# Optimization experiments

Measured on AMD Instinct MI355X. Metric: run time of the kernel, lower is better.

Reference implementation:

```python
import jax, jax.numpy as jnp
import numpy as np

H = 32        # num query heads
KVH = 8       # num kv heads
HD = 64       # head dim
G = H // KVH  # GQA group size
THETA = 10000.0


def _rope(x, pos):
    # x: [B, h, S, HD], pos: [B, S] int
    inv_freq = 1.0 / (THETA ** (jnp.arange(0, HD, 2, dtype=jnp.float32) / HD))  # [HD/2]
    freqs = pos.astype(jnp.float32)[:, :, None] * inv_freq[None, None, :]        # [B, S, HD/2]
    emb = jnp.concatenate([freqs, freqs], axis=-1)                               # [B, S, HD]
    cos = jnp.cos(emb)[:, None, :, :].astype(x.dtype)                            # [B, 1, S, HD]
    sin = jnp.sin(emb)[:, None, :, :].astype(x.dtype)
    x1, x2 = x[..., : HD // 2], x[..., HD // 2 :]
    rot = jnp.concatenate([-x2, x1], axis=-1)
    return x * cos + rot * sin


def setup_inputs() -> dict:
    key = jax.random.key(0)
    ks = jax.random.split(key, 8)
    B, S, D = 2, 2048, 2048
    s = 0.02
    hidden_states = jax.random.normal(ks[0], (B, S, D), dtype=jnp.float32)
    position_ids = jnp.broadcast_to(jnp.arange(S, dtype=jnp.int32)[None, :], (B, S))
    Wq = jax.random.normal(ks[1], (H * HD, D), dtype=jnp.float32) * s
    bq = jax.random.normal(ks[2], (H * HD,), dtype=jnp.float32) * s
    Wk = jax.random.normal(ks[3], (KVH * HD, D), dtype=jnp.float32) * s
    bk = jax.random.normal(ks[4], (KVH * HD,), dtype=jnp.float32) * s
    Wv = jax.random.normal(ks[5], (KVH * HD, D), dtype=jnp.float32) * s
    bv = jax.random.normal(ks[6], (KVH * HD,), dtype=jnp.float32) * s
    Wo = jax.random.normal(ks[7], (D, H * HD), dtype=jnp.float32) * s
    return dict(hidden_states=hidden_states, position_ids=position_ids,
                Wq=Wq, bq=bq, Wk=Wk, bk=bk, Wv=Wv, bv=bv, Wo=Wo)


def reference(hidden_states, position_ids, Wq, bq, Wk, bk, Wv, bv, Wo):
    B, S, D = hidden_states.shape
    scale = 1.0 / np.sqrt(HD)
    q = hidden_states @ Wq.T + bq  # [B, S, H*HD]
    k = hidden_states @ Wk.T + bk  # [B, S, KVH*HD]
    v = hidden_states @ Wv.T + bv
    q = q.reshape(B, S, H, HD).transpose(0, 2, 1, 3)      # [B, H, S, HD]
    k = k.reshape(B, S, KVH, HD).transpose(0, 2, 1, 3)    # [B, KVH, S, HD]
    v = v.reshape(B, S, KVH, HD).transpose(0, 2, 1, 3)
    q = _rope(q, position_ids)
    k = _rope(k, position_ids)
    # GQA: view q as [B, KVH, G, S, HD]; equivalent math to repeat_kv of k/v
    qg = q.reshape(B, KVH, G, S, HD)
    scores = jnp.einsum('bkgqd,bkld->bkgql', qg, k) * scale  # [B, KVH, G, S, S]
    # causal mask (past_seq_len = 0)
    causal = jnp.tril(jnp.ones((S, S), dtype=bool))
    scores = jnp.where(causal[None, None, None, :, :], scores, jnp.float32(-jnp.inf))
    attn = jax.nn.softmax(scores.astype(jnp.float32), axis=-1).astype(q.dtype)
    out = jnp.einsum('bkgql,bkld->bkgqd', attn, v)            # [B, KVH, G, S, HD]
    out = out.reshape(B, H, S, HD).transpose(0, 2, 1, 3).reshape(B, S, H * HD)
    return out @ Wo.T
```

## Files before the change

### kernel.cpp

```cpp
#include <hip/hip_runtime.h>
#include <hip/hip_bf16.h>

typedef unsigned short u16;
typedef __bf16 bf16x8 __attribute__((ext_vector_type(8)));
typedef float f32x4 __attribute__((ext_vector_type(4)));
typedef float f32x16 __attribute__((ext_vector_type(16)));
typedef float f32x4v __attribute__((ext_vector_type(4)));
typedef unsigned short u16x4 __attribute__((ext_vector_type(4)));
typedef unsigned int u32x4 __attribute__((ext_vector_type(4)));

__device__ __forceinline__ u16 f2bf(float f) {
  __bf16 h = (__bf16)f;
  return __builtin_bit_cast(unsigned short, h);
}

__device__ __forceinline__ f32x16 z16() {
  f32x16 z;
#pragma unroll
  for (int i = 0; i < 16; ++i) z[i] = 0.f;
  return z;
}

__device__ __forceinline__ int permh(int ph) {
  int blk = ph >> 4;
  int pblk = (blk == 1) ? 2 : ((blk == 2) ? 1 : blk);
  return (pblk << 4) | (ph & 15);
}

__device__ __forceinline__ int SW(int r, int c) {
  return (r << 6) + (c ^ ((r & 7) << 3));
}

#define GLOAD_LDS16(gp, lp) __builtin_amdgcn_global_load_lds( \
    (const __attribute__((address_space(1))) unsigned int*)(gp), \
    (__attribute__((address_space(3))) unsigned int*)(lp), 16, 0, 0)

#define BAR() do { asm volatile("" ::: "memory"); __builtin_amdgcn_s_barrier(); asm volatile("" ::: "memory"); } while (0)
#define VMCNT(n) asm volatile("s_waitcnt vmcnt(" #n ")" ::: "memory")
#define LG0() asm volatile("s_waitcnt lgkmcnt(0)" ::: "memory")
#define SBAR0() __builtin_amdgcn_sched_barrier(0)

__global__ void prep_all(const f32x4v* __restrict__ hs, u16x4* __restrict__ hsb,
                         const f32x4v* __restrict__ wq, const f32x4v* __restrict__ wk,
                         const f32x4v* __restrict__ wv, u16x4* __restrict__ wqkvb,
                         const f32x4v* __restrict__ wo, u16x4* __restrict__ wob,
                         const int* __restrict__ pos, float* __restrict__ cosT,
                         float* __restrict__ sinT, const float* __restrict__ bq,
                         const float* __restrict__ bk, const float* __restrict__ bv,
                         float* __restrict__ bc) {
  int i = blockIdx.x * 256 + threadIdx.x;
  if (i < 2097152) {
    f32x4v v = hs[i];
    u16x4 o; o.x = f2bf(v.x); o.y = f2bf(v.y); o.z = f2bf(v.z); o.w = f2bf(v.w);
    hsb[i] = o;
  } else if (i < 3670016) {
    int j = i - 2097152;
    int row = j >> 9, c4 = j & 511;
    f32x4v v;
    if (row < 2048) {
      int sr = (row & ~63) | permh(row & 63);
      v = wq[(size_t)sr * 512 + c4];
    } else if (row < 2560) {
      int rk = row - 2048;
      int sr = (rk & ~63) | permh(rk & 63);
      v = wk[(size_t)sr * 512 + c4];
    } else {
      v = wv[(size_t)(row - 2560) * 512 + c4];
    }
    u16x4 o; o.x = f2bf(v.x); o.y = f2bf(v.y); o.z = f2bf(v.z); o.w = f2bf(v.w);
    wqkvb[j] = o;
  } else if (i < 4718592) {
    int j = i - 3670016;
    f32x4v v = wo[j];
    u16x4 o; o.x = f2bf(v.x); o.y = f2bf(v.y); o.z = f2bf(v.z); o.w = f2bf(v.w);
    wob[j] = o;
  } else if (i < 4849664) {
    int j = i - 4718592;
    int bs = j >> 5, f = j & 31;
    float inv = exp2f(-(float)f * (13.287712379549449f / 32.f));
    float ang = (float)pos[bs] * inv;
    cosT[j] = cosf(ang);
    sinT[j] = sinf(ang);
  } else if (i < 4852736) {
    int j = i - 4849664;
    float v;
    if (j < 2048) {
      v = bq[(j & ~63) | permh(j & 63)];
    } else if (j < 2560) {
      int jk = j - 2048;
      v = bk[(jk & ~63) | permh(jk & 63)];
    } else {
      v = bv[j - 2560];
    }
    bc[j] = v;
  }
}

#define STAGE_A(kt, hh) { \
    const u16* s_ = aS + (size_t)(hh) * (BM / 2) * K + (size_t)(kt) * 64; \
    u16* d_ = lds + ((kt) & 1) * BUF + (hh) * (BM * 32) + wid * 512; \
    GLOAD_LDS16(s_, d_); \
    if constexpr (BM == 256) GLOAD_LDS16(s_ + (size_t)64 * K, d_ + 4096); \
  }

#define STAGE_B(kt, hh) { \
    const u16* s_ = bS + (size_t)(hh) * 128 * K + (size_t)(kt) * 64; \
    u16* d_ = lds + ((kt) & 1) * BUF + BM * 64 + (hh) * 8192 + wid * 512; \
    GLOAD_LDS16(s_, d_); \
    GLOAD_LDS16(s_ + (size_t)64 * K, d_ + 4096); \
  }

#define LDA8(buf, qm) { \
    const u16* p_ = lds + (buf) * BUF + ((qm) * (BM / 2) + arow) * 64; \
    _Pragma("unroll") \
    for (int mf = 0; mf < MF; ++mf) { \
      af[mf][0] = *(const bf16x8*)(p_ + mf * 1024 + koff0); \
      af[mf][1] = *(const bf16x8*)(p_ + mf * 1024 + koff1); \
    } }

#define LDB8(buf, qn) { \
    const u16* p_ = lds + (buf) * BUF + BM * 64 + ((qn) * 128 + brow) * 64; \
    _Pragma("unroll") \
    for (int nf = 0; nf < 2; ++nf) { \
      bfr[nf][0] = *(const bf16x8*)(p_ + nf * 1024 + koff0); \
      bfr[nf][1] = *(const bf16x8*)(p_ + nf * 1024 + koff1); \
    } }

#define MM8(qm, qn) { \
    __builtin_amdgcn_s_setprio(1); \
    _Pragma("unroll") \
    for (int mf = 0; mf < MF; ++mf) \
      _Pragma("unroll") \
      for (int nf = 0; nf < 2; ++nf) { \
        acc[(qm) * MF + mf][(qn) * 2 + nf] = __builtin_amdgcn_mfma_f32_16x16x32_bf16( \
            af[mf][0], bfr[nf][0], acc[(qm) * MF + mf][(qn) * 2 + nf], 0, 0, 0); \
        acc[(qm) * MF + mf][(qn) * 2 + nf] = __builtin_amdgcn_mfma_f32_16x16x32_bf16( \
            af[mf][1], bfr[nf][1], acc[(qm) * MF + mf][(qn) * 2 + nf], 0, 0, 0); \
      } \
    __builtin_amdgcn_s_setprio(0); }

#define VMCNT_GATE() do { if constexpr (BM == 256) { VMCNT(6); } else { VMCNT(4); } } while (0)

template <int MODE, int BM>
__global__ __launch_bounds__(512, 2) void gemm8(
    const u16* __restrict__ A, const u16* __restrict__ Bw, const int K, const int N,
    u16* __restrict__ qb, u16* __restrict__ kb, u16* __restrict__ vtb,
    const float* __restrict__ biasc, const float* __restrict__ cosT,
    const float* __restrict__ sinT, float* __restrict__ outf) {
  constexpr int MF = BM / 64;
  constexpr int BUF = BM * 64 + 16384;
  __shared__ u16 lds[2 * BUF];
  const int tid = threadIdx.x;
  const int lane = tid & 63, wid = tid >> 6;
  const int wr = wid >> 2, wc = wid & 3;
  const int col = lane & 15, rg = lane >> 4;
  const int tm = blockIdx.x, tn = blockIdx.y;

  const int srow = tid >> 3;
  const int scol = ((tid & 7) ^ (srow & 7)) * 8;
  const u16* aS = A + ((size_t)tm * BM + srow) * K + scol;
  const u16* bS = Bw + ((size_t)tn * 256 + srow) * K + scol;

  const int koff0 = (rg ^ (col & 7)) * 8;
  const int koff1 = ((4 + rg) ^ (col & 7)) * 8;
  const int arow = wr * (BM / 4) + col;
  const int brow = wc * 32 + col;

  f32x4 acc[2 * MF][4];
#pragma unroll
  for (int i = 0; i < 2 * MF; ++i)
#pragma unroll
    for (int j = 0; j < 4; ++j) acc[i][j] = (f32x4){0.f, 0.f, 0.f, 0.f};
  bf16x8 af[MF][2], bfr[2][2];

  const int ITERS = K >> 7;

  STAGE_A(0, 0); STAGE_A(0, 1);
  STAGE_B(0, 0); STAGE_B(0, 1);
  STAGE_A(1, 0); STAGE_B(1, 1); STAGE_A(1, 1);
  VMCNT_GATE();
  BAR();

#pragma unroll 1
  for (int it = 0; it < ITERS; ++it) {
    const int t0 = it * 2;
    const bool more = (it + 1 < ITERS);
    LDA8(0, 0); LDB8(0, 0);
    STAGE_B(t0 + 1, 0);
    MM8(0, 0); SBAR0(); BAR();
    LDB8(0, 1);
    if (more) STAGE_A(t0 + 2, 0);
    MM8(0, 1); SBAR0(); BAR();
    LDA8(0, 1);
    if (more) STAGE_B(t0 + 2, 1);
    MM8(1, 1); SBAR0(); BAR();
    LDB8(0, 0);
    if (more) STAGE_A(t0 + 2, 1);
    MM8(1, 0); SBAR0();
    if (more) { VMCNT_GATE(); } else { VMCNT(0); }
    BAR();
    LDA8(1, 0); LDB8(1, 0);
    if (more) STAGE_B(t0 + 2, 0);
    MM8(0, 0); SBAR0(); BAR();
    LDB8(1, 1);
    if (more) STAGE_A(t0 + 3, 0);
    MM8(0, 1); SBAR0(); BAR();
    LDA8(1, 1);
    if (more) STAGE_B(t0 + 3, 1);
    MM8(1, 1); SBAR0(); BAR();
    LDB8(1, 0);
    if (more) STAGE_A(t0 + 3, 1);
    MM8(1, 0); SBAR0();
    if (more) VMCNT_GATE();
    BAR();
  }

  if constexpr (MODE == 1) {
#pragma unroll
    for (int qm = 0; qm < 2; ++qm)
#pragma unroll
      for (int mf = 0; mf < MF; ++mf) {
        const int mbase = tm * BM + qm * (BM / 2) + wr * (BM / 4) + mf * 16 + rg * 4;
#pragma unroll
        for (int qn = 0; qn < 2; ++qn)
#pragma unroll
          for (int nf = 0; nf < 2; ++nf) {
            const int n = tn * 256 + qn * 128 + wc * 32 + nf * 16 + col;
#pragma unroll
            for (int r = 0; r < 4; ++r)
              outf[(size_t)(mbase + r) * N + n] = acc[qm * MF + mf][qn * 2 + nf][r];
          }
      }
  } else {
    if (tn < 8) {
      const float QS = 0.18033688011112042f;
#pragma unroll
      for (int qm = 0; qm < 2; ++qm)
#pragma unroll
        for (int qn = 0; qn < 2; ++qn) {
          const int h = tn * 4 + qn * 2 + (wc >> 1);
          const int c32 = wc & 1;
          const int n0 = tn * 256 + qn * 128 + wc * 32 + col;
          const float b1 = biasc[n0], b2 = biasc[n0 + 16];
          const int f = c32 * 16 + col;
          const int ph0 = c32 * 32 + col;
#pragma unroll
          for (int mf = 0; mf < MF; ++mf)
#pragma unroll
            for (int r = 0; r < 4; ++r) {
              const int m = tm * 256 + qm * 128 + wr * 64 + mf * 16 + rg * 4 + r;
              const int b = m >> 11, s = m & 2047;
              const size_t base = ((size_t)(b * 32 + h) * 2048 + s) * 64;
              float x1 = acc[qm * MF + mf][qn * 2 + 0][r] + b1;
              float x2 = acc[qm * MF + mf][qn * 2 + 1][r] + b2;
              float c = cosT[m * 32 + f], sn = sinT[m * 32 + f];
              qb[base + ph0]      = f2bf((x1 * c - x2 * sn) * QS);
              qb[base + ph0 + 16] = f2bf((x2 * c + x1 * sn) * QS);
            }
        }
    } else if (tn < 10) {
#pragma unroll
      for (int qm = 0; qm < 2; ++qm)
#pragma unroll
        for (int qn = 0; qn < 2; ++qn) {
          const int hk = (tn - 8) * 4 + qn * 2 + (wc >> 1);
          const int c32 = wc & 1;
          const int n0 = tn * 256 + qn * 128 + wc * 32 + col;
          const float b1 = biasc[n0], b2 = biasc[n0 + 16];
          const int f = c32 * 16 + col;
          const int ph0 = c32 * 32 + col;
#pragma unroll
          for (int mf = 0; mf < MF; ++mf)
#pragma unroll
            for (int r = 0; r < 4; ++r) {
              const int m = tm * 256 + qm * 128 + wr * 64 + mf * 16 + rg * 4 + r;
              const int b = m >> 11, s = m & 2047;
              const size_t base = ((size_t)(b * 8 + hk) * 2048 + s) * 64;
              float x1 = acc[qm * MF + mf][qn * 2 + 0][r] + b1;
              float x2 = acc[qm * MF + mf][qn * 2 + 1][r] + b2;
              float c = cosT[m * 32 + f], sn = sinT[m * 32 + f];
              kb[base + ph0]      = f2bf(x1 * c - x2 * sn);
              kb[base + ph0 + 16] = f2bf(x2 * c + x1 * sn);
            }
        }
    } else {
#pragma unroll
      for (int qm = 0; qm < 2; ++qm)
#pragma unroll
        for (int qn = 0; qn < 2; ++qn)
#pragma unroll
          for (int nf = 0; nf < 2; ++nf) {
            const int n = tn * 256 + qn * 128 + wc * 32 + nf * 16 + col;
            const int hk = (n - 2560) >> 6;
            const int d = (n - 2560) & 63;
            const float bvv = biasc[n];
#pragma unroll
            for (int mf = 0; mf < MF; ++mf)
#pragma unroll
              for (int r = 0; r < 4; ++r) {
                const int m = tm * 256 + qm * 128 + wr * 64 + mf * 16 + rg * 4 + r;
                const int b = m >> 11, s = m & 2047;
                vtb[((size_t)(b * 8 + hk) * 64 + d) * 2048 + s] =
                    f2bf(acc[qm * MF + mf][qn * 2 + nf][r] + bvv);
              }
          }
    }
  }
}

#define RSTAGE_A(kt, c) GLOAD_LDS16( \
    aS + (size_t)((c) * 64) * K + (size_t)(kt) * 64, \
    lds + ((kt) & 1) * BUFSZ + (c) * 4096 + tid * 8)

#define RSTAGE_B(kt, c) GLOAD_LDS16( \
    bS + (size_t)((c) * 64) * K + (size_t)(kt) * 64, \
    lds + ((kt) & 1) * BUFSZ + 16384 + (c) * 4096 + tid * 8)

#define STAGE_H1(kt) { RSTAGE_A(kt, 0); RSTAGE_A(kt, 1); RSTAGE_A(kt, 2); }
#define STAGE_H2(kt) { RSTAGE_A(kt, 3); RSTAGE_B(kt, 0); RSTAGE_B(kt, 1); }

#define RLDA(dst, buf, kof) { \
    const u16* p_ = lds + (buf) * BUFSZ + arow * 64; \
    _Pragma("unroll") \
    for (int mf = 0; mf < 4; ++mf) dst[mf] = *(const bf16x8*)(p_ + mf * 1024 + (kof)); }

#define RLDB(dst, buf, kof) { \
    const u16* p_ = lds + (buf) * BUFSZ + 16384 + brow * 64; \
    _Pragma("unroll") \
    for (int nf = 0; nf < 4; ++nf) dst[nf] = *(const bf16x8*)(p_ + nf * 1024 + (kof)); }

#define RMM(afs, bfs) { \
    __builtin_amdgcn_s_setprio(1); \
    _Pragma("unroll") \
    for (int mf = 0; mf < 4; ++mf) \
      _Pragma("unroll") \
      for (int nf = 0; nf < 4; ++nf) \
        acc[mf][nf] = __builtin_amdgcn_mfma_f32_16x16x32_bf16(afs[mf], bfs[nf], acc[mf][nf], 0, 0, 0); \
    __builtin_amdgcn_s_setprio(0); }

__global__ void __launch_bounds__(512)
__attribute__((amdgpu_waves_per_eu(2, 2)))
gemm_o(const u16* __restrict__ A, const u16* __restrict__ Bw, const int K, const int N,
       float* __restrict__ outf) {
  constexpr int BUFSZ = (256 + 128) * 64;
  __shared__ u16 lds[2 * BUFSZ];
  const int tid = threadIdx.x;
  const int lane = tid & 63, wid = tid >> 6;
  const int wr = wid >> 1, wc = wid & 1;
  const int col = lane & 15, rg = lane >> 4;
  const int tm = blockIdx.x, tn = blockIdx.y;

  const int srow = tid >> 3;
  const int scol = ((tid & 7) ^ (srow & 7)) * 8;
  const u16* aS = A + ((size_t)tm * 256 + srow) * K + scol;
  const u16* bS = Bw + ((size_t)tn * 128 + srow) * K + scol;

  const int koff0 = (rg ^ (col & 7)) * 8;
  const int koff1 = ((4 + rg) ^ (col & 7)) * 8;
  const int arow = wr * 64 + col;
  const int brow = wc * 64 + col;

  f32x4 acc[4][4];
#pragma unroll
  for (int i = 0; i < 4; ++i)
#pragma unroll
    for (int j = 0; j < 4; ++j) acc[i][j] = (f32x4){0.f, 0.f, 0.f, 0.f};
  bf16x8 aX[4], aY[4], bA[4], bB[4];

  const int ITERS = K >> 7;

  STAGE_H1(0); STAGE_H2(0); STAGE_H1(1); STAGE_H2(1);
  VMCNT(6);
  BAR();
  RLDA(aX, 0, koff0); RLDB(bA, 0, koff0);

#pragma unroll 1
  for (int it = 0; it < ITERS; ++it) {
    const bool more = (it + 1 < ITERS);
    if (it > 0) STAGE_H2(2 * it + 1);
    RLDA(aY, 0, koff1); RLDB(bB, 0, koff1);
    RMM(aX, bA);
    LG0(); VMCNT(0); BAR();
    if (more) STAGE_H1(2 * it + 2);
    RLDA(aX, 1, koff0); RLDB(bA, 1, koff0);
    RMM(aY, bB);
    LG0(); BAR();
    if (more) STAGE_H2(2 * it + 2);
    RLDA(aY, 1, koff1); RLDB(bB, 1, koff1);
    RMM(aX, bA);
    LG0();
    if (more) VMCNT(0);
    BAR();
    if (more) {
      STAGE_H1(2 * it + 3);
      RLDA(aX, 0, koff0); RLDB(bA, 0, koff0);
    }
    RMM(aY, bB);
    LG0(); BAR();
  }

#pragma unroll
  for (int mf = 0; mf < 4; ++mf) {
    const int mbase = tm * 256 + wr * 64 + mf * 16 + rg * 4;
#pragma unroll
    for (int nf = 0; nf < 4; ++nf) {
      const int n = tn * 128 + wc * 64 + nf * 16 + col;
#pragma unroll
      for (int r = 0; r < 4; ++r)
        outf[(size_t)(mbase + r) * N + n] = acc[mf][nf][r];
    }
  }
}

__global__ __launch_bounds__(256, 4) void attn_k(
    const u16* __restrict__ qb, const u16* __restrict__ kb,
    const u16* __restrict__ vtb, u16* __restrict__ attb) {
  __shared__ __align__(16) u16 Kl[3][2048];
  __shared__ __align__(16) u16 Vl[3][2048];
  const int tid = threadIdx.x, lane = tid & 63, w = tid >> 6;
  const int q32 = lane & 31, hl = lane >> 5, h4 = hl * 4;

  const int bid = blockIdx.x;
  const int xcd = bid & 7, pos = bid >> 3;
  const int grp = xcd * 8 + (pos >> 4);
  const int s0 = pos & 15;
  const int strip = ((pos >> 5) & 1) ? (15 - s0) : s0;
  const int h = grp & 31, b = grp >> 5;
  const int qb0 = (15 - strip) * 128;
  const int hk = h >> 2;
  const int q0w = qb0 + w * 32;

  const u16* Qp = qb + ((size_t)(b * 32 + h) * 2048 + q0w + q32) * 64 + hl * 8;
  bf16x8 qf[4];
#pragma unroll
  for (int s = 0; s < 4; ++s) qf[s] = *(const bf16x8*)(Qp + s * 16);

  f32x16 po[2];
  po[0] = z16(); po[1] = z16();
  float l_part = 0.f;

  const u16* Kbase = kb + (size_t)(b * 8 + hk) * 2048 * 64;
  const u16* Vbase = vtb + (size_t)(b * 8 + hk) * 64 * 2048;
  const int srow = tid >> 3, c8 = (tid & 7) << 3;
  const int cs = c8 ^ ((srow & 7) << 3);
  const u16* Ksrc = Kbase + (size_t)srow * 64 + cs;
  const u16* Vsrc = Vbase + (size_t)(srow * 2 + (cs >> 5)) * 2048 + (cs & 31);
  char* Kdst0 = (char*)Kl + w * 1024;
  char* Vdst0 = (char*)Vl + w * 1024;

  const int nkv = (qb0 >> 5) + 4;
  const int rowmax = q0w + 31;

  GLOAD_LDS16(Ksrc, Kdst0);
  GLOAD_LDS16(Vsrc, Vdst0);
  GLOAD_LDS16(Ksrc + 2048, Kdst0 + 4096);
  GLOAD_LDS16(Vsrc + 32, Vdst0 + 4096);

  for (int it = 0; it < nkv; ++it) {
    const int kv0 = it * 32;
    const int buf = it % 3;
    if (it + 2 < nkv) {
      const int b2 = (it + 2) % 3;
      GLOAD_LDS16(Ksrc + (size_t)(it + 2) * 2048, Kdst0 + b2 * 4096);
      GLOAD_LDS16(Vsrc + (size_t)(it + 2) * 32, Vdst0 + b2 * 4096);
      VMCNT(4);
    } else if (it + 1 < nkv) {
      VMCNT(2);
    } else {
      VMCNT(0);
    }
    BAR();

    if (kv0 <= rowmax) {
      const u16* Kb = (const u16*)((const char*)Kl + buf * 4096);
      const u16* Vb = (const u16*)((const char*)Vl + buf * 4096);
      const bool diag = (kv0 + 32 > q0w);

      f32x16 t = z16();
#pragma unroll
      for (int s = 0; s < 4; ++s) {
        bf16x8 kf = *(const bf16x8*)&Kb[SW(q32, s * 16 + hl * 8)];
        t = __builtin_amdgcn_mfma_f32_32x32x16_bf16(kf, qf[s], t, 0, 0, 0);
      }
      if (diag) {
        const int qg = q0w + q32;
#pragma unroll
        for (int r = 0; r < 16; ++r) {
          const int kvg = kv0 + (r & 3) + 8 * (r >> 2) + h4;
          if (kvg > qg) t[r] = -1e30f;
        }
      }
#pragma unroll
      for (int r = 0; r < 16; ++r) t[r] = __builtin_amdgcn_exp2f(t[r]);
      l_part += (((t[0] + t[1]) + (t[2] + t[3])) + ((t[4] + t[5]) + (t[6] + t[7]))) +
                (((t[8] + t[9]) + (t[10] + t[11])) + ((t[12] + t[13]) + (t[14] + t[15])));

      unsigned pw0, pw1, pw2, pw3, pw4, pw5, pw6, pw7;
      asm("v_cvt_pk_bf16_f32 %0, %1, %2" : "=v"(pw0) : "v"(t[0]), "v"(t[1]));
      asm("v_cvt_pk_bf16_f32 %0, %1, %2" : "=v"(pw1) : "v"(t[2]), "v"(t[3]));
      asm("v_cvt_pk_bf16_f32 %0, %1, %2" : "=v"(pw2) : "v"(t[4]), "v"(t[5]));
      asm("v_cvt_pk_bf16_f32 %0, %1, %2" : "=v"(pw3) : "v"(t[6]), "v"(t[7]));
      asm("v_cvt_pk_bf16_f32 %0, %1, %2" : "=v"(pw4) : "v"(t[8]), "v"(t[9]));
      asm("v_cvt_pk_bf16_f32 %0, %1, %2" : "=v"(pw5) : "v"(t[10]), "v"(t[11]));
      asm("v_cvt_pk_bf16_f32 %0, %1, %2" : "=v"(pw6) : "v"(t[12]), "v"(t[13]));
      asm("v_cvt_pk_bf16_f32 %0, %1, %2" : "=v"(pw7) : "v"(t[14]), "v"(t[15]));
      asm("v_permlane32_swap_b32 %0, %1" : "+v"(pw0), "+v"(pw2));
      asm("v_permlane32_swap_b32 %0, %1" : "+v"(pw1), "+v"(pw3));
      asm("v_permlane32_swap_b32 %0, %1" : "+v"(pw4), "+v"(pw6));
      asm("v_permlane32_swap_b32 %0, %1" : "+v"(pw5), "+v"(pw7));
      const bf16x8 pa0 = __builtin_bit_cast(bf16x8, (u32x4){pw0, pw1, pw2, pw3});
      const bf16x8 pa1 = __builtin_bit_cast(bf16x8, (u32x4){pw4, pw5, pw6, pw7});

      __builtin_amdgcn_s_setprio(1);
#pragma unroll
      for (int dblk = 0; dblk < 2; ++dblk) {
        const int d = dblk * 32 + q32;
        const int vr = d >> 1, vc = (d & 1) * 32 + hl * 8;
        bf16x8 v0 = *(const bf16x8*)&Vb[SW(vr, vc)];
        bf16x8 v1 = *(const bf16x8*)&Vb[SW(vr, vc + 16)];
        po[dblk] = __builtin_amdgcn_mfma_f32_32x32x16_bf16(pa0, v0, po[dblk], 0, 0, 0);
        po[dblk] = __builtin_amdgcn_mfma_f32_32x32x16_bf16(pa1, v1, po[dblk], 0, 0, 0);
      }
      __builtin_amdgcn_s_setprio(0);
    }
    SBAR0();
    BAR();
  }

  const float l_full = l_part + __shfl_xor(l_part, 32);
#pragma unroll
  for (int r = 0; r < 16; ++r) {
    const int qrl = (r & 3) + 8 * (r >> 2) + h4;
    const float lq = __shfl(l_full, qrl);
    const float inv = 1.f / lq;
    const size_t base = ((size_t)b * 2048 + q0w + qrl) * 2048 + h * 64;
    attb[base + q32]      = f2bf(po[0][r] * inv);
    attb[base + 32 + q32] = f2bf(po[1][r] * inv);
  }
}

extern "C" void kernel_launch(void* const* d_in, const int* in_sizes, int n_in,
                              void* d_out, int out_size, void* d_ws, size_t ws_size,
                              hipStream_t stream) {
  const float* hs = (const float*)d_in[0];
  const int* pos = (const int*)d_in[1];
  const float* Wq = (const float*)d_in[2];
  const float* bq = (const float*)d_in[3];
  const float* Wk = (const float*)d_in[4];
  const float* bk = (const float*)d_in[5];
  const float* Wv = (const float*)d_in[6];
  const float* bv = (const float*)d_in[7];
  const float* Wo = (const float*)d_in[8];
  float* out = (float*)d_out;

  char* ws = (char*)d_ws;
  size_t off = 0;
  u16* hsb = (u16*)(ws + off);   off += (size_t)4096 * 2048 * 2;
  u16* wqkvb = (u16*)(ws + off); off += (size_t)3072 * 2048 * 2;
  u16* wob = (u16*)(ws + off);   off += (size_t)2048 * 2048 * 2;
  float* biasc = (float*)(ws + off); off += 3072 * 4;
  float* cosT = (float*)(ws + off);  off += (size_t)4096 * 32 * 4;
  float* sinT = (float*)(ws + off);  off += (size_t)4096 * 32 * 4;
  u16* qb = (u16*)(ws + off);    off += (size_t)2 * 32 * 2048 * 64 * 2;
  u16* kb = (u16*)(ws + off);    off += (size_t)2 * 8 * 2048 * 64 * 2;
  u16* vtb = (u16*)(ws + off);   off += (size_t)2 * 8 * 64 * 2048 * 2;
  u16* attb = (u16*)(ws + off);  off += (size_t)4096 * 2048 * 2;

  prep_all<<<18956, 256, 0, stream>>>((const f32x4v*)hs, (u16x4*)hsb,
                                      (const f32x4v*)Wq, (const f32x4v*)Wk,
                                      (const f32x4v*)Wv, (u16x4*)wqkvb,
                                      (const f32x4v*)Wo, (u16x4*)wob,
                                      pos, cosT, sinT, bq, bk, bv, biasc);

  gemm8<0, 256><<<dim3(16, 12), 512, 0, stream>>>(hsb, wqkvb, 2048, 3072,
                                                  qb, kb, vtb, biasc, cosT, sinT, nullptr);
  attn_k<<<1024, 256, 0, stream>>>(qb, kb, vtb, attb);
  gemm_o<<<dim3(16, 16), 512, 0, stream>>>(attb, wob, 2048, 2048, out);
}
```

Before: 172.2 us.

## Read K and V directly from global memory instead of shared-memory staging

The attention kernel stops staging K/V tiles into triple-buffered LDS with async global-to-LDS loads and barriers. Each wave now loads its K and V fragments straight from global memory and runs only the KV tiles its causal range needs. This removes block-wide barriers and LDS traffic and lets waves advance independently. In exchange, the four waves in a block no longer share a K/V tile, so global/L2 traffic grows, and the loads have no explicit prefetch to hide latency.

Result: slower. 240.5 us (+39.7%).

```diff
diff --git a/kernel.cpp b/kernel.cpp
--- a/kernel.cpp
+++ b/kernel.cpp
@@ -25,10 +25,6 @@
   int blk = ph >> 4;
   int pblk = (blk == 1) ? 2 : ((blk == 2) ? 1 : blk);
   return (pblk << 4) | (ph & 15);
-}
-
-__device__ __forceinline__ int SW(int r, int c) {
-  return (r << 6) + (c ^ ((r & 7) << 3));
 }
 
 #define GLOAD_LDS16(gp, lp) __builtin_amdgcn_global_load_lds( \
@@ -415,8 +411,6 @@
 __global__ __launch_bounds__(256, 4) void attn_k(
     const u16* __restrict__ qb, const u16* __restrict__ kb,
     const u16* __restrict__ vtb, u16* __restrict__ attb) {
-  __shared__ __align__(16) u16 Kl[3][2048];
-  __shared__ __align__(16) u16 Vl[3][2048];
   const int tid = threadIdx.x, lane = tid & 63, w = tid >> 6;
   const int q32 = lane & 31, hl = lane >> 5, h4 = hl * 4;
 
@@ -439,92 +433,60 @@
   po[0] = z16(); po[1] = z16();
   float l_part = 0.f;
 
-  const u16* Kbase = kb + (size_t)(b * 8 + hk) * 2048 * 64;
-  const u16* Vbase = vtb + (size_t)(b * 8 + hk) * 64 * 2048;
-  const int srow = tid >> 3, c8 = (tid & 7) << 3;
-  const int cs = c8 ^ ((srow & 7) << 3);
-  const u16* Ksrc = Kbase + (size_t)srow * 64 + cs;
-  const u16* Vsrc = Vbase + (size_t)(srow * 2 + (cs >> 5)) * 2048 + (cs & 31);
-  char* Kdst0 = (char*)Kl + w * 1024;
-  char* Vdst0 = (char*)Vl + w * 1024;
-
-  const int nkv = (qb0 >> 5) + 4;
-  const int rowmax = q0w + 31;
-
-  GLOAD_LDS16(Ksrc, Kdst0);
-  GLOAD_LDS16(Vsrc, Vdst0);
-  GLOAD_LDS16(Ksrc + 2048, Kdst0 + 4096);
-  GLOAD_LDS16(Vsrc + 32, Vdst0 + 4096);
-
-  for (int it = 0; it < nkv; ++it) {
+  const u16* Kp = kb + (size_t)(b * 8 + hk) * 2048 * 64 + (size_t)q32 * 64 + hl * 8;
+  const u16* Vp = vtb + (size_t)(b * 8 + hk) * 64 * 2048 + (size_t)q32 * 2048 + hl * 8;
+
+  const int ntiles = (q0w >> 5) + 1;
+
+  for (int it = 0; it < ntiles; ++it) {
     const int kv0 = it * 32;
-    const int buf = it % 3;
-    if (it + 2 < nkv) {
-      const int b2 = (it + 2) % 3;
-      GLOAD_LDS16(Ksrc + (size_t)(it + 2) * 2048, Kdst0 + b2 * 4096);
-      GLOAD_LDS16(Vsrc + (size_t)(it + 2) * 32, Vdst0 + b2 * 4096);
-      VMCNT(4);
-    } else if (it + 1 < nkv) {
-      VMCNT(2);
-    } else {
-      VMCNT(0);
-    }
-    BAR();
-
-    if (kv0 <= rowmax) {
-      const u16* Kb = (const u16*)((const char*)Kl + buf * 4096);
-      const u16* Vb = (const u16*)((const char*)Vl + buf * 4096);
-      const bool diag = (kv0 + 32 > q0w);
-
-      f32x16 t = z16();
-#pragma unroll
-      for (int s = 0; s < 4; ++s) {
-        bf16x8 kf = *(const bf16x8*)&Kb[SW(q32, s * 16 + hl * 8)];
-        t = __builtin_amdgcn_mfma_f32_32x32x16_bf16(kf, qf[s], t, 0, 0, 0);
+    const bool diag = (it == ntiles - 1);
+
+    f32x16 t = z16();
+#pragma unroll
+    for (int s = 0; s < 4; ++s) {
+      bf16x8 kf = *(const bf16x8*)(Kp + (size_t)kv0 * 64 + s * 16);
+      t = __builtin_amdgcn_mfma_f32_32x32x16_bf16(kf, qf[s], t, 0, 0, 0);
+    }
+    if (diag) {
+      const int qg = q0w + q32;
+#pragma unroll
+      for (int r = 0; r < 16; ++r) {
+        const int kvg = kv0 + (r & 3) + 8 * (r >> 2) + h4;
+        if (kvg > qg) t[r] = -1e30f;
       }
-      if (diag) {
-        const int qg = q0w + q32;
-#pragma unroll
-        for (int r = 0; r < 16; ++r) {
-          const int kvg = kv0 + (r & 3) + 8 * (r >> 2) + h4;
-          if (kvg > qg) t[r] = -1e30f;
-        }
-      }
-#pragma unroll
-      for (int r = 0; r < 16; ++r) t[r] = __builtin_amdgcn_exp2f(t[r]);
-      l_part += (((t[0] + t[1]) + (t[2] + t[3])) + ((t[4] + t[5]) + (t[6] + t[7]))) +
-                (((t[8] + t[9]) + (t[10] + t[11])) + ((t[12] + t[13]) + (t[14] + t[15])));
-
-      unsigned pw0, pw1, pw2, pw3, pw4, pw5, pw6, pw7;
-      asm("v_cvt_pk_bf16_f32 %0, %1, %2" : "=v"(pw0) : "v"(t[0]), "v"(t[1]));
-      asm("v_cvt_pk_bf16_f32 %0, %1, %2" : "=v"(pw1) : "v"(t[2]), "v"(t[3]));
-      asm("v_cvt_pk_bf16_f32 %0, %1, %2" : "=v"(pw2) : "v"(t[4]), "v"(t[5]));
-      asm("v_cvt_pk_bf16_f32 %0, %1, %2" : "=v"(pw3) : "v"(t[6]), "v"(t[7]));
-      asm("v_cvt_pk_bf16_f32 %0, %1, %2" : "=v"(pw4) : "v"(t[8]), "v"(t[9]));
-      asm("v_cvt_pk_bf16_f32 %0, %1, %2" : "=v"(pw5) : "v"(t[10]), "v"(t[11]));
-      asm("v_cvt_pk_bf16_f32 %0, %1, %2" : "=v"(pw6) : "v"(t[12]), "v"(t[13]));
-      asm("v_cvt_pk_bf16_f32 %0, %1, %2" : "=v"(pw7) : "v"(t[14]), "v"(t[15]));
-      asm("v_permlane32_swap_b32 %0, %1" : "+v"(pw0), "+v"(pw2));
-      asm("v_permlane32_swap_b32 %0, %1" : "+v"(pw1), "+v"(pw3));
-      asm("v_permlane32_swap_b32 %0, %1" : "+v"(pw4), "+v"(pw6));
-      asm("v_permlane32_swap_b32 %0, %1" : "+v"(pw5), "+v"(pw7));
-      const bf16x8 pa0 = __builtin_bit_cast(bf16x8, (u32x4){pw0, pw1, pw2, pw3});
-      const bf16x8 pa1 = __builtin_bit_cast(bf16x8, (u32x4){pw4, pw5, pw6, pw7});
-
-      __builtin_amdgcn_s_setprio(1);
-#pragma unroll
-      for (int dblk = 0; dblk < 2; ++dblk) {
-        const int d = dblk * 32 + q32;
-        const int vr = d >> 1, vc = (d & 1) * 32 + hl * 8;
-        bf16x8 v0 = *(const bf16x8*)&Vb[SW(vr, vc)];
-        bf16x8 v1 = *(const bf16x8*)&Vb[SW(vr, vc + 16)];
-        po[dblk] = __builtin_amdgcn_mfma_f32_32x32x16_bf16(pa0, v0, po[dblk], 0, 0, 0);
-        po[dblk] = __builtin_amdgcn_mfma_f32_32x32x16_bf16(pa1, v1, po[dblk], 0, 0, 0);
-      }
-      __builtin_amdgcn_s_setprio(0);
-    }
-    SBAR0();
-    BAR();
+    }
+#pragma unroll
+    for (int r = 0; r < 16; ++r) t[r] = __builtin_amdgcn_exp2f(t[r]);
+    l_part += (((t[0] + t[1]) + (t[2] + t[3])) + ((t[4] + t[5]) + (t[6] + t[7]))) +
+              (((t[8] + t[9]) + (t[10] + t[11])) + ((t[12] + t[13]) + (t[14] + t[15])));
+
+    unsigned pw0, pw1, pw2, pw3, pw4, pw5, pw6, pw7;
+    asm("v_cvt_pk_bf16_f32 %0, %1, %2" : "=v"(pw0) : "v"(t[0]), "v"(t[1]));
+    asm("v_cvt_pk_bf16_f32 %0, %1, %2" : "=v"(pw1) : "v"(t[2]), "v"(t[3]));
+    asm("v_cvt_pk_bf16_f32 %0, %1, %2" : "=v"(pw2) : "v"(t[4]), "v"(t[5]));
+    asm("v_cvt_pk_bf16_f32 %0, %1, %2" : "=v"(pw3) : "v"(t[6]), "v"(t[7]));
+    asm("v_cvt_pk_bf16_f32 %0, %1, %2" : "=v"(pw4) : "v"(t[8]), "v"(t[9]));
+    asm("v_cvt_pk_bf16_f32 %0, %1, %2" : "=v"(pw5) : "v"(t[10]), "v"(t[11]));
+    asm("v_cvt_pk_bf16_f32 %0, %1, %2" : "=v"(pw6) : "v"(t[12]), "v"(t[13]));
+    asm("v_cvt_pk_bf16_f32 %0, %1, %2" : "=v"(pw7) : "v"(t[14]), "v"(t[15]));
+    asm("v_permlane32_swap_b32 %0, %1" : "+v"(pw0), "+v"(pw2));
+    asm("v_permlane32_swap_b32 %0, %1" : "+v"(pw1), "+v"(pw3));
+    asm("v_permlane32_swap_b32 %0, %1" : "+v"(pw4), "+v"(pw6));
+    asm("v_permlane32_swap_b32 %0, %1" : "+v"(pw5), "+v"(pw7));
+    const bf16x8 pa0 = __builtin_bit_cast(bf16x8, (u32x4){pw0, pw1, pw2, pw3});
+    const bf16x8 pa1 = __builtin_bit_cast(bf16x8, (u32x4){pw4, pw5, pw6, pw7});
+
+    __builtin_amdgcn_s_setprio(1);
+#pragma unroll
+    for (int dblk = 0; dblk < 2; ++dblk) {
+      const u16* vp = Vp + (size_t)dblk * 32 * 2048 + kv0;
+      bf16x8 v0 = *(const bf16x8*)(vp);
+      bf16x8 v1 = *(const bf16x8*)(vp + 16);
+      po[dblk] = __builtin_amdgcn_mfma_f32_32x32x16_bf16(pa0, v0, po[dblk], 0, 0, 0);
+      po[dblk] = __builtin_amdgcn_mfma_f32_32x32x16_bf16(pa1, v1, po[dblk], 0, 0, 0);
+    }
+    __builtin_amdgcn_s_setprio(0);
   }
 
   const float l_full = l_part + __shfl_xor(l_part, 32);
```

## Process two KV tiles per barrier step with double-buffered tile pairs

Applied to the files above, without the earlier changes.

Restructures the attention main loop so each iteration loads and computes a pair of 32-wide KV tiles. The triple-buffered single-tile ring becomes a double-buffered ring of tile pairs, and the per-tile work moves into a macro. This halves the number of workgroup barriers and wait points per KV element, giving more independent MFMA work between syncs. In exchange LDS use rises from 24KB to 32KB per block, which may limit occupancy at 4 blocks per CU.

New measurement: 171.7 us (median of 2 runs). Within noise of the previous version (-0.3%).

```diff
diff --git a/kernel.cpp b/kernel.cpp
--- a/kernel.cpp
+++ b/kernel.cpp
@@ -412,11 +412,59 @@
   }
 }
 
+#define ATTN_TILE(kv0v, Kb, Vb) { \
+      const bool diag = ((kv0v) + 32 > q0w); \
+      f32x16 t = z16(); \
+      _Pragma("unroll") \
+      for (int s = 0; s < 4; ++s) { \
+        bf16x8 kf = *(const bf16x8*)&(Kb)[SW(q32, s * 16 + hl * 8)]; \
+        t = __builtin_amdgcn_mfma_f32_32x32x16_bf16(kf, qf[s], t, 0, 0, 0); \
+      } \
+      if (diag) { \
+        const int qg = q0w + q32; \
+        _Pragma("unroll") \
+        for (int r = 0; r < 16; ++r) { \
+          const int kvg = (kv0v) + (r & 3) + 8 * (r >> 2) + h4; \
+          if (kvg > qg) t[r] = -1e30f; \
+        } \
+      } \
+      _Pragma("unroll") \
+      for (int r = 0; r < 16; ++r) t[r] = __builtin_amdgcn_exp2f(t[r]); \
+      l_part += (((t[0] + t[1]) + (t[2] + t[3])) + ((t[4] + t[5]) + (t[6] + t[7]))) + \
+                (((t[8] + t[9]) + (t[10] + t[11])) + ((t[12] + t[13]) + (t[14] + t[15]))); \
+      unsigned pw0, pw1, pw2, pw3, pw4, pw5, pw6, pw7; \
+      asm("v_cvt_pk_bf16_f32 %0, %1, %2" : "=v"(pw0) : "v"(t[0]), "v"(t[1])); \
+      asm("v_cvt_pk_bf16_f32 %0, %1, %2" : "=v"(pw1) : "v"(t[2]), "v"(t[3])); \
+      asm("v_cvt_pk_bf16_f32 %0, %1, %2" : "=v"(pw2) : "v"(t[4]), "v"(t[5])); \
+      asm("v_cvt_pk_bf16_f32 %0, %1, %2" : "=v"(pw3) : "v"(t[6]), "v"(t[7])); \
+      asm("v_cvt_pk_bf16_f32 %0, %1, %2" : "=v"(pw4) : "v"(t[8]), "v"(t[9])); \
+      asm("v_cvt_pk_bf16_f32 %0, %1, %2" : "=v"(pw5) : "v"(t[10]), "v"(t[11])); \
+      asm("v_cvt_pk_bf16_f32 %0, %1, %2" : "=v"(pw6) : "v"(t[12]), "v"(t[13])); \
+      asm("v_cvt_pk_bf16_f32 %0, %1, %2" : "=v"(pw7) : "v"(t[14]), "v"(t[15])); \
+      asm("v_permlane32_swap_b32 %0, %1" : "+v"(pw0), "+v"(pw2)); \
+      asm("v_permlane32_swap_b32 %0, %1" : "+v"(pw1), "+v"(pw3)); \
+      asm("v_permlane32_swap_b32 %0, %1" : "+v"(pw4), "+v"(pw6)); \
+      asm("v_permlane32_swap_b32 %0, %1" : "+v"(pw5), "+v"(pw7)); \
+      const bf16x8 pa0 = __builtin_bit_cast(bf16x8, (u32x4){pw0, pw1, pw2, pw3}); \
+      const bf16x8 pa1 = __builtin_bit_cast(bf16x8, (u32x4){pw4, pw5, pw6, pw7}); \
+      __builtin_amdgcn_s_setprio(1); \
+      _Pragma("unroll") \
+      for (int dblk = 0; dblk < 2; ++dblk) { \
+        const int d = dblk * 32 + q32; \
+        const int vr = d >> 1, vc = (d & 1) * 32 + hl * 8; \
+        bf16x8 v0 = *(const bf16x8*)&(Vb)[SW(vr, vc)]; \
+        bf16x8 v1 = *(const bf16x8*)&(Vb)[SW(vr, vc + 16)]; \
+        po[dblk] = __builtin_amdgcn_mfma_f32_32x32x16_bf16(pa0, v0, po[dblk], 0, 0, 0); \
+        po[dblk] = __builtin_amdgcn_mfma_f32_32x32x16_bf16(pa1, v1, po[dblk], 0, 0, 0); \
+      } \
+      __builtin_amdgcn_s_setprio(0); \
+    }
+
 __global__ __launch_bounds__(256, 4) void attn_k(
     const u16* __restrict__ qb, const u16* __restrict__ kb,
     const u16* __restrict__ vtb, u16* __restrict__ attb) {
-  __shared__ __align__(16) u16 Kl[3][2048];
-  __shared__ __align__(16) u16 Vl[3][2048];
+  __shared__ __align__(16) u16 Kl[2][2][2048];
+  __shared__ __align__(16) u16 Vl[2][2][2048];
   const int tid = threadIdx.x, lane = tid & 63, w = tid >> 6;
   const int q32 = lane & 31, hl = lane >> 5, h4 = hl * 4;
 
@@ -449,6 +497,7 @@
   char* Vdst0 = (char*)Vl + w * 1024;
 
   const int nkv = (qb0 >> 5) + 4;
+  const int npairs = nkv >> 1;
   const int rowmax = q0w + 31;
 
   GLOAD_LDS16(Ksrc, Kdst0);
@@ -456,73 +505,30 @@
   GLOAD_LDS16(Ksrc + 2048, Kdst0 + 4096);
   GLOAD_LDS16(Vsrc + 32, Vdst0 + 4096);
 
-  for (int it = 0; it < nkv; ++it) {
-    const int kv0 = it * 32;
-    const int buf = it % 3;
-    if (it + 2 < nkv) {
-      const int b2 = (it + 2) % 3;
-      GLOAD_LDS16(Ksrc + (size_t)(it + 2) * 2048, Kdst0 + b2 * 4096);
-      GLOAD_LDS16(Vsrc + (size_t)(it + 2) * 32, Vdst0 + b2 * 4096);
+  for (int p = 0; p < npairs; ++p) {
+    const int slot = p & 1;
+    if (p + 1 < npairs) {
+      const int s1 = (p + 1) & 1;
+      const int t0 = 2 * p + 2;
+      GLOAD_LDS16(Ksrc + (size_t)t0 * 2048, Kdst0 + s1 * 8192);
+      GLOAD_LDS16(Vsrc + (size_t)t0 * 32, Vdst0 + s1 * 8192);
+      GLOAD_LDS16(Ksrc + (size_t)(t0 + 1) * 2048, Kdst0 + s1 * 8192 + 4096);
+      GLOAD_LDS16(Vsrc + (size_t)(t0 + 1) * 32, Vdst0 + s1 * 8192 + 4096);
       VMCNT(4);
-    } else if (it + 1 < nkv) {
-      VMCNT(2);
     } else {
       VMCNT(0);
     }
     BAR();
 
-    if (kv0 <= rowmax) {
-      const u16* Kb = (const u16*)((const char*)Kl + buf * 4096);
-      const u16* Vb = (const u16*)((const char*)Vl + buf * 4096);
-      const bool diag = (kv0 + 32 > q0w);
-
-      f32x16 t = z16();
-#pragma unroll
-      for (int s = 0; s < 4; ++s) {
-        bf16x8 kf = *(const bf16x8*)&Kb[SW(q32, s * 16 + hl * 8)];
-        t = __builtin_amdgcn_mfma_f32_32x32x16_bf16(kf, qf[s], t, 0, 0, 0);
-      }
-      if (diag) {
-        const int qg = q0w + q32;
-#pragma unroll
-        for (int r = 0; r < 16; ++r) {
-          const int kvg = kv0 + (r & 3) + 8 * (r >> 2) + h4;
-          if (kvg > qg) t[r] = -1e30f;
-        }
-      }
-#pragma unroll
-      for (int r = 0; r < 16; ++r) t[r] = __builtin_amdgcn_exp2f(t[r]);
-      l_part += (((t[0] + t[1]) + (t[2] + t[3])) + ((t[4] + t[5]) + (t[6] + t[7]))) +
-                (((t[8] + t[9]) + (t[10] + t[11])) + ((t[12] + t[13]) + (t[14] + t[15])));
-
-      unsigned pw0, pw1, pw2, pw3, pw4, pw5, pw6, pw7;
-      asm("v_cvt_pk_bf16_f32 %0, %1, %2" : "=v"(pw0) : "v"(t[0]), "v"(t[1]));
-      asm("v_cvt_pk_bf16_f32 %0, %1, %2" : "=v"(pw1) : "v"(t[2]), "v"(t[3]));
-      asm("v_cvt_pk_bf16_f32 %0, %1, %2" : "=v"(pw2) : "v"(t[4]), "v"(t[5]));
-      asm("v_cvt_pk_bf16_f32 %0, %1, %2" : "=v"(pw3) : "v"(t[6]), "v"(t[7]));
-      asm("v_cvt_pk_bf16_f32 %0, %1, %2" : "=v"(pw4) : "v"(t[8]), "v"(t[9]));
-      asm("v_cvt_pk_bf16_f32 %0, %1, %2" : "=v"(pw5) : "v"(t[10]), "v"(t[11]));
-      asm("v_cvt_pk_bf16_f32 %0, %1, %2" : "=v"(pw6) : "v"(t[12]), "v"(t[13]));
-      asm("v_cvt_pk_bf16_f32 %0, %1, %2" : "=v"(pw7) : "v"(t[14]), "v"(t[15]));
-      asm("v_permlane32_swap_b32 %0, %1" : "+v"(pw0), "+v"(pw2));
-      asm("v_permlane32_swap_b32 %0, %1" : "+v"(pw1), "+v"(pw3));
-      asm("v_permlane32_swap_b32 %0, %1" : "+v"(pw4), "+v"(pw6));
-      asm("v_permlane32_swap_b32 %0, %1" : "+v"(pw5), "+v"(pw7));
-      const bf16x8 pa0 = __builtin_bit_cast(bf16x8, (u32x4){pw0, pw1, pw2, pw3});
-      const bf16x8 pa1 = __builtin_bit_cast(bf16x8, (u32x4){pw4, pw5, pw6, pw7});
-
-      __builtin_amdgcn_s_setprio(1);
-#pragma unroll
-      for (int dblk = 0; dblk < 2; ++dblk) {
-        const int d = dblk * 32 + q32;
-        const int vr = d >> 1, vc = (d & 1) * 32 + hl * 8;
-        bf16x8 v0 = *(const bf16x8*)&Vb[SW(vr, vc)];
-        bf16x8 v1 = *(const bf16x8*)&Vb[SW(vr, vc + 16)];
-        po[dblk] = __builtin_amdgcn_mfma_f32_32x32x16_bf16(pa0, v0, po[dblk], 0, 0, 0);
-        po[dblk] = __builtin_amdgcn_mfma_f32_32x32x16_bf16(pa1, v1, po[dblk], 0, 0, 0);
-      }
-      __builtin_amdgcn_s_setprio(0);
-    }
+    const int kvA = 2 * p * 32;
+    const int kvB = kvA + 32;
+    const u16* KbA = &Kl[slot][0][0];
+    const u16* VbA = &Vl[slot][0][0];
+    if (kvA <= rowmax) ATTN_TILE(kvA, KbA, VbA);
+    const u16* KbB = &Kl[slot][1][0];
+    const u16* VbB = &Vl[slot][1][0];
+    if (kvB <= rowmax) ATTN_TILE(kvB, KbB, VbB);
+
     SBAR0();
     BAR();
   }
```
